# Kernel optimization log

Hardware: AMD Instinct MI355X
Metric: run time of the kernel (lower is better)

## Reference

```python
import jax, jax.numpy as jnp
import numpy as np

G = 16                 # grid side -> 4096 voxels
N_GRID = G ** 3
N_NODES = 4096         # protein nodes
DEG = 256              # node neighbors per grid voxel
HID = 64               # MPNN hidden == ResNet in_channels
NUM_CLASSES = 20
BN = np.float32(1.0 / np.sqrt(1.0 + 1e-5))  # eval-mode BatchNorm3d (mean=0, var=1, gamma=1, beta=0)


def _lin(key, fi, fo):
    return jax.random.normal(key, (fi, fo), jnp.float32) * (fi ** -0.5)


def _cw(key, o, i, k):
    return jax.random.normal(key, (o, i, k, k, k), jnp.float32) * ((i * k ** 3) ** -0.5)


def setup_inputs() -> dict:
    key = jax.random.key(0)
    ks = jax.random.split(key, 32)
    n_edges = N_GRID * DEG
    # every grid voxel receives exactly DEG messages (bincount never zero)
    edge_i = jax.random.randint(ks[0], (n_edges,), 0, N_NODES, dtype=jnp.int32)
    edge_j = jnp.repeat(jnp.arange(N_GRID, dtype=jnp.int32), DEG)
    edge_index = jnp.stack([edge_i, edge_j])  # [2, E]

    node_embedding = jax.random.normal(ks[1], (N_NODES, HID), jnp.float32)
    node_pos = jax.random.uniform(ks[2], (N_NODES, 3), jnp.float32)
    gx = (jnp.arange(G, dtype=jnp.float32) + 0.5) / G
    gd, gh, gw = jnp.meshgrid(gx, gx, gx, indexing='ij')
    grid_pos = jnp.stack([gd, gh, gw], -1).reshape(N_GRID, 3)

    z = lambda n: jnp.zeros((n,), jnp.float32)
    return {
        'node_embedding': node_embedding, 'node_pos': node_pos,
        'grid_pos': grid_pos, 'edge_index': edge_index,
        # MPNN edge / message / update MLPs
        'ew1': _lin(ks[3], 6, HID), 'eb1': z(HID), 'ew2': _lin(ks[4], HID, HID), 'eb2': z(HID),
        'mw1': _lin(ks[5], 2 * HID, HID), 'mb1': z(HID), 'mw2': _lin(ks[6], HID, HID), 'mb2': z(HID),
        'uw1': _lin(ks[7], HID, HID), 'ub1': z(HID), 'uw2': _lin(ks[8], HID, HID), 'ub2': z(HID),
        # ResNet3D: 3 Blocks (conv3 a, conv3 b, conv5 shortcut) with channels 64->64, 64->128, 128->256
        'c1a': _cw(ks[9], 64, 64, 3), 'c1b': _cw(ks[10], 64, 64, 3), 'c1s': _cw(ks[11], 64, 64, 5),
        'c2a': _cw(ks[12], 128, 64, 3), 'c2b': _cw(ks[13], 128, 128, 3), 'c2s': _cw(ks[14], 128, 64, 5),
        'c3a': _cw(ks[15], 256, 128, 3), 'c3b': _cw(ks[16], 256, 256, 3), 'c3s': _cw(ks[17], 256, 128, 5),
        'fcw': _lin(ks[18], 256, NUM_CLASSES), 'fcb': z(NUM_CLASSES),
    }


def _mlp(x, w1, b1, w2, b2):
    return jax.nn.silu(x @ w1 + b1) @ w2 + b2


def _conv(x, w, p):
    return jax.lax.conv_general_dilated(
        x, w, window_strides=(1, 1, 1), padding=[(p, p)] * 3,
        dimension_numbers=('NCDHW', 'OIDHW', 'NCDHW'))


def _block(x, wa, wb, ws):
    out = jax.nn.relu(_conv(x, wa, 1) * BN)
    out = _conv(out, wb, 1) * BN
    sc = _conv(x, ws, 2) * BN
    return jax.nn.relu(out + sc)


def reference(node_embedding, node_pos, grid_pos, edge_index,
              ew1, eb1, ew2, eb2, mw1, mb1, mw2, mb2, uw1, ub1, uw2, ub2,
              c1a, c1b, c1s, c2a, c2b, c2s, c3a, c3b, c3s, fcw, fcb):
    i, j = edge_index[0], edge_index[1]
    # ---- MPNN: gather, edge MLP, message MLP, scatter-mean, update MLP ----
    edge_attr = jnp.concatenate([node_pos[i], grid_pos[j]], axis=-1)        # [E, 6]
    pos_emb = _mlp(edge_attr, ew1, eb1, ew2, eb2)                           # [E, H]
    msg = _mlp(jnp.concatenate([node_embedding[i], pos_emb], -1),
               mw1, mb1, mw2, mb2)                                          # [E, H]
    agg = jax.ops.segment_sum(msg, j, num_segments=N_GRID)                  # [N_GRID, H]
    cnt = jax.ops.segment_sum(jnp.ones((msg.shape[0],), msg.dtype), j,
                              num_segments=N_GRID)
    grid_feat = _mlp(agg / cnt[:, None], uw1, ub1, uw2, ub2)                # [N_GRID, H]
    # ---- ResNet3D over the grid volume ----
    x = grid_feat.T.reshape(1, HID, G, G, G) * BN                           # instance_norm1 (eval BN)
    x = _block(x, c1a, c1b, c1s)
    x = _block(x, c2a, c2b, c2s)
    x = _block(x, c3a, c3b, c3s)
    pooled = jnp.max(x, axis=(2, 3, 4))                                     # max_pool3d(kernel=spatial)
    return pooled @ fcw + fcb                                               # [1, NUM_CLASSES]
```

## Files before the change

kernel.cpp:

```cpp
#include <hip/hip_runtime.h>
#include <math.h>

#define BN_S 0.9999950000374997f

typedef _Float16 half8 __attribute__((ext_vector_type(8)));
typedef float f32x4 __attribute__((ext_vector_type(4)));

__device__ __forceinline__ float silu_f(float x) {
    return __fdividef(x, 1.0f + __expf(-x));
}

__device__ __forceinline__ void gld16(const void* g, void* l) {
    __builtin_amdgcn_global_load_lds(
        (const __attribute__((address_space(1))) void*)g,
        (__attribute__((address_space(3))) void*)l, 16, 0, 0);
}

__global__ __launch_bounds__(64) void prep_w_k(
    const float* __restrict__ ew2, const float* __restrict__ mw1,
    const float* __restrict__ mw2, const float* __restrict__ uw1,
    const float* __restrict__ mb2, const float* __restrict__ ub1,
    float* __restrict__ W_mu, float* __restrict__ b_mu,
    _Float16* __restrict__ wemt_h, _Float16* __restrict__ wemt_l)
{
    const int k = blockIdx.x, c = threadIdx.x;
    float s = 0.f;
    for (int m = 0; m < 64; m++) s = fmaf(ew2[k*64 + m], mw1[(64 + m)*64 + c], s);
    {
        const int q = k >> 5, kg = (k >> 3) & 3, jj = k & 7;
        const int sl = q*256 + c*4 + kg;
        const int p = sl ^ ((sl >> 3) & 7);
        const _Float16 h = (_Float16)s;
        const _Float16 l = (_Float16)(s - (float)h);
        wemt_h[p*8 + jj] = h;
        wemt_l[p*8 + jj] = l;
    }
    float s2 = 0.f;
    for (int m = 0; m < 64; m++) s2 = fmaf(mw2[k*64 + m], uw1[m*64 + c], s2);
    W_mu[k*64 + c] = s2;
    if (k == 0) {
        float s3 = ub1[c];
        for (int m = 0; m < 64; m++) s3 = fmaf(mb2[m], uw1[m*64 + c], s3);
        b_mu[c] = s3;
    }
}

__global__ __launch_bounds__(64) void prep_nodes_k(
    const float* __restrict__ node_embedding, const float* __restrict__ node_pos,
    const float* __restrict__ grid_pos, const float* __restrict__ ew1,
    const float* __restrict__ eb1, const float* __restrict__ mw1,
    const float* __restrict__ mb1, const float* __restrict__ eb2,
    float* __restrict__ a_node, float* __restrict__ g_vox, float* __restrict__ n_node)
{
    const int v = blockIdx.x, c = threadIdx.x;
    const float p0 = node_pos[v*3], p1 = node_pos[v*3 + 1], p2 = node_pos[v*3 + 2];
    a_node[v*64 + c] = fmaf(p0, ew1[c], fmaf(p1, ew1[64 + c], fmaf(p2, ew1[128 + c], eb1[c])));
    const float q0 = grid_pos[v*3], q1 = grid_pos[v*3 + 1], q2 = grid_pos[v*3 + 2];
    g_vox[v*64 + c] = fmaf(q0, ew1[192 + c], fmaf(q1, ew1[256 + c], q2 * ew1[320 + c]));
    float s = mb1[c];
    for (int k = 0; k < 64; k++) s = fmaf(node_embedding[v*64 + k], mw1[k*64 + c], s);
    for (int k = 0; k < 64; k++) s = fmaf(eb2[k], mw1[(64 + k)*64 + c], s);
    n_node[v*64 + c] = s;
}

template<int K3, int NCOG, int NCH>
__global__ __launch_bounds__(256) void wsplit_k(
    const float* __restrict__ w, _Float16* __restrict__ dh, _Float16* __restrict__ dl,
    int CI)
{
    __shared__ float s[32*K3];
    const int co = blockIdx.x, cig = blockIdx.y, t = threadIdx.x;
    const float* src = w + ((size_t)co*CI + cig*32)*K3;
    for (int m = t; m < 32*K3; m += 256) s[m] = src[m];
    __syncthreads();
    const int coG = co >> 6, col = co & 63;
    for (int m = t; m < 32*K3; m += 256) {
        const int tap = m >> 5, cil = m & 31;
        const float x = s[cil*K3 + tap];
        const _Float16 h = (_Float16)x;
        const _Float16 l = (_Float16)(x - (float)h);
        const int b = cil >> 3, jj = cil & 7;
        const int sl = col*4 + b;
        const int p = sl ^ ((sl >> 3) & 7);
        const size_t base = ((size_t)(tap*NCOG + coG)*NCH + cig) * 2048;
        dh[base + p*8 + jj] = h;
        dl[base + p*8 + jj] = l;
    }
}

__global__ __launch_bounds__(256) void edge_kernel(
    const int* __restrict__ edge_i,
    const float* __restrict__ a_node, const float* __restrict__ g_vox,
    const float* __restrict__ n_node,
    const _Float16* __restrict__ wemt_h, const _Float16* __restrict__ wemt_l,
    const float* __restrict__ W_mu, const float* __restrict__ b_mu,
    const float* __restrict__ uw2, const float* __restrict__ ub2,
    _Float16* __restrict__ x0h, _Float16* __restrict__ x0l)
{
    __shared__ __align__(16) _Float16 sAh[4096], sAl[4096];
    __shared__ __align__(16) _Float16 sBh[4096], sBl[4096];
    __shared__ float sV1[64], sV2[64];

    const int j = blockIdx.x, t = threadIdx.x;
    const int lane = t & 63, wv = t >> 6, ln15 = lane & 15, kg = lane >> 4;
    const int ebase = j << 8;

    gld16(wemt_h + t*8, &sAh[t*8]);
    gld16(wemt_h + 2048 + t*8, &sAh[2048 + t*8]);
    gld16(wemt_l + t*8, &sAl[t*8]);
    gld16(wemt_l + 2048 + t*8, &sAl[2048 + t*8]);

    const int r = t >> 2, sub = t & 3;
    float gv[16];
    #pragma unroll
    for (int m = 0; m < 16; m++) gv[m] = g_vox[j*64 + sub*16 + m];

    asm volatile("s_waitcnt vmcnt(0)" ::: "memory");
    __syncthreads();

    float psum[4] = {0.f, 0.f, 0.f, 0.f};

    for (int T = 0; T < 4; T++) {
        {
            const int i = edge_i[ebase + T*64 + r];
            float s1[16];
            #pragma unroll
            for (int m = 0; m < 16; m++)
                s1[m] = silu_f(a_node[i*64 + sub*16 + m] + gv[m]);
            half8 h0, l0, h1, l1;
            #pragma unroll
            for (int m = 0; m < 8; m++) {
                h0[m] = (_Float16)s1[m];
                l0[m] = (_Float16)(s1[m] - (float)h0[m]);
                h1[m] = (_Float16)s1[8 + m];
                l1[m] = (_Float16)(s1[8 + m] - (float)h1[m]);
            }
            const int q = sub >> 1, kg0 = (sub & 1) * 2;
            const int slot0 = (q*4 + kg0)*64 + r;
            *(half8*)&sBh[slot0*8] = h0; *(half8*)&sBl[slot0*8] = l0;
            *(half8*)&sBh[(slot0 + 64)*8] = h1; *(half8*)&sBl[(slot0 + 64)*8] = l1;
        }
        __syncthreads();
        #pragma unroll
        for (int eF = 0; eF < 4; eF++) {
            const int e = eF*16 + ln15;
            const int ie = edge_i[ebase + T*64 + e];
            f32x4 acc;
            {
                const float4 nv = *(const float4*)&n_node[(size_t)ie*64 + wv*16 + kg*4];
                acc[0] = nv.x; acc[1] = nv.y; acc[2] = nv.z; acc[3] = nv.w;
            }
            #pragma unroll
            for (int q = 0; q < 2; q++) {
                const int sa = q*256 + (wv*16 + ln15)*4 + kg;
                const int pa = sa ^ ((sa >> 3) & 7);
                const half8 Ah = *(const half8*)&sAh[pa*8];
                const half8 Al = *(const half8*)&sAl[pa*8];
                const int sb = ((q*4 + kg)*64 + e)*8;
                const half8 Bh = *(const half8*)&sBh[sb];
                const half8 Bl = *(const half8*)&sBl[sb];
                acc = __builtin_amdgcn_mfma_f32_16x16x32_f16(Ah, Bh, acc, 0, 0, 0);
                acc = __builtin_amdgcn_mfma_f32_16x16x32_f16(Ah, Bl, acc, 0, 0, 0);
                acc = __builtin_amdgcn_mfma_f32_16x16x32_f16(Al, Bh, acc, 0, 0, 0);
            }
            #pragma unroll
            for (int rg = 0; rg < 4; rg++) psum[rg] += silu_f(acc[rg]);
        }
        __syncthreads();
    }

    #pragma unroll
    for (int rg = 0; rg < 4; rg++) {
        float v = psum[rg];
        v += __shfl_xor(v, 1, 64); v += __shfl_xor(v, 2, 64);
        v += __shfl_xor(v, 4, 64); v += __shfl_xor(v, 8, 64);
        psum[rg] = v;
    }
    if (ln15 == 0) {
        #pragma unroll
        for (int rg = 0; rg < 4; rg++)
            sV1[wv*16 + kg*4 + rg] = psum[rg] * (1.0f / 256.0f);
    }
    __syncthreads();
    if (t < 64) {
        float h = b_mu[t];
        for (int k = 0; k < 64; k++) h = fmaf(sV1[k], W_mu[k*64 + t], h);
        sV2[t] = silu_f(h);
    }
    __syncthreads();
    if (t < 64) {
        float g = ub2[t];
        for (int k = 0; k < 64; k++) g = fmaf(sV2[k], uw2[k*64 + t], g);
        const float val = g * BN_S;
        const _Float16 hh = (_Float16)val;
        const _Float16 ll = (_Float16)(val - (float)hh);
        const int c = t, zz = j >> 8, v = j & 255;
        const size_t a16 = ((size_t)((c >> 5)*16 + zz)*1024 + ((c >> 3) & 3)*256 + v)*8 + (c & 7);
        x0h[a16] = hh; x0l[a16] = ll;
    }
}

template<int KK, int CI, int NCOG, int CIS>
__global__ __launch_bounds__(256) void conv_mfma_k(
    const _Float16* __restrict__ xh, const _Float16* __restrict__ xl,
    const _Float16* __restrict__ wh, const _Float16* __restrict__ wl,
    float* __restrict__ slab)
{
    constexpr int P = KK/2, K2 = KK*KK, NCH = CI/32, NCHS = NCH/CIS, CO = NCOG*64;
    const int d0 = blockIdx.x, coG = blockIdx.y;
    const int cis = blockIdx.z / KK, kd = blockIdx.z % KK;
    const int t = threadIdx.x;
    const int lane = t & 63, wv = t >> 6;
    const int ln15 = lane & 15, kg = lane >> 4;

    float* sout = slab + ((size_t)blockIdx.z*CO + coG*64)*4096 + d0*256;
    const int z = d0 + kd - P;
    if ((unsigned)z >= 16u) {
        for (int m = t; m < 64*256; m += 256)
            sout[(size_t)(m >> 8)*4096 + (m & 255)] = 0.f;
        return;
    }

    __shared__ __align__(16) _Float16 sXh[2][8192];
    __shared__ __align__(16) _Float16 sXl[2][8192];
    __shared__ __align__(16) _Float16 zb[8];
    if (t < 8) zb[t] = (_Float16)0.f;

    int aoff[4];
    #pragma unroll
    for (int cf = 0; cf < 4; cf++) {
        const int s = (cf*16 + ln15)*4 + kg;
        aoff[cf] = (s ^ ((s >> 3) & 7)) * 8;
    }

    auto stage_X = [&](int xb, int ch) {
        const size_t b16 = ((size_t)ch*16 + z) * 8192;
        #pragma unroll
        for (int q = 0; q < 4; q++) {
            gld16(xh + b16 + (q*256 + t)*8, &sXh[xb][(q*256 + t)*8]);
            gld16(xl + b16 + (q*256 + t)*8, &sXl[xb][(q*256 + t)*8]);
        }
    };
    auto loadA = [&](int ch, int t2, half8* Ah, half8* Al) {
        const size_t b = ((size_t)((kd*K2 + t2)*NCOG + coG)*NCH + ch) * 2048;
        #pragma unroll
        for (int cf = 0; cf < 4; cf++) {
            Ah[cf] = *(const half8*)&wh[b + aoff[cf]];
            Al[cf] = *(const half8*)&wl[b + aoff[cf]];
        }
    };

    f32x4 acc[4][4];
    #pragma unroll
    for (int a = 0; a < 4; a++)
        #pragma unroll
        for (int b = 0; b < 4; b++)
            #pragma unroll
            for (int r2 = 0; r2 < 4; r2++) acc[a][b][r2] = 0.f;

    const int ch0 = cis * NCHS;
    half8 nAh[4], nAl[4];
    stage_X(0, ch0);
    loadA(ch0, 0, nAh, nAl);
    asm volatile("s_waitcnt vmcnt(0)" ::: "memory");
    __syncthreads();

    for (int cc = 0; cc < NCHS; cc++) {
        const int ch = ch0 + cc, xb = cc & 1;
        if (cc + 1 < NCHS) stage_X(xb ^ 1, ch + 1);
        for (int t2 = 0; t2 < K2; t2++) {
            half8 cAh[4], cAl[4];
            #pragma unroll
            for (int cf = 0; cf < 4; cf++) { cAh[cf] = nAh[cf]; cAl[cf] = nAl[cf]; }
            if (t2 + 1 < K2)          loadA(ch, t2 + 1, nAh, nAl);
            else if (cc + 1 < NCHS)   loadA(ch + 1, 0, nAh, nAl);

            const int kh = t2 / KK, kw = t2 % KK;
            __builtin_amdgcn_s_setprio(1);
            #pragma unroll
            for (int f = 0; f < 4; f++) {
                const int h_in = wv*4 + f + kh - P;
                if ((unsigned)h_in < 16u) {
                    const int w_in = ln15 + kw - P;
                    const bool ok = (unsigned)w_in < 16u;
                    const int slot = ok ? (kg*256 + h_in*16 + w_in) : 0;
                    const half8 Bh = ok ? *(const half8*)&sXh[xb][slot*8] : *(const half8*)zb;
                    const half8 Bl = ok ? *(const half8*)&sXl[xb][slot*8] : *(const half8*)zb;
                    #pragma unroll
                    for (int cf = 0; cf < 4; cf++) {
                        acc[cf][f] = __builtin_amdgcn_mfma_f32_16x16x32_f16(cAh[cf], Bh, acc[cf][f], 0, 0, 0);
                        acc[cf][f] = __builtin_amdgcn_mfma_f32_16x16x32_f16(cAh[cf], Bl, acc[cf][f], 0, 0, 0);
                        acc[cf][f] = __builtin_amdgcn_mfma_f32_16x16x32_f16(cAl[cf], Bh, acc[cf][f], 0, 0, 0);
                    }
                }
            }
            __builtin_amdgcn_s_setprio(0);
        }
        __syncthreads();
    }

    #pragma unroll
    for (int cf = 0; cf < 4; cf++)
        #pragma unroll
        for (int f = 0; f < 4; f++)
            #pragma unroll
            for (int r2 = 0; r2 < 4; r2++)
                sout[(size_t)(cf*16 + kg*4 + r2)*4096 + wv*64 + f*16 + ln15] = acc[cf][f][r2];
}

template<int S, int RMODE, int OUT>
__global__ __launch_bounds__(256) void reduce_k(
    const float* __restrict__ pbuf, const float* __restrict__ addsrc,
    float* __restrict__ outf, _Float16* __restrict__ oh, _Float16* __restrict__ ol,
    int CO)
{
    const int z = blockIdx.x, c8 = blockIdx.y, v = threadIdx.x;
    float val[8];
    #pragma unroll
    for (int jj = 0; jj < 8; jj++) {
        const int c = c8*8 + jj;
        float a = 0.f;
        #pragma unroll
        for (int s = 0; s < S; s++)
            a += pbuf[((size_t)s*CO + c)*4096 + z*256 + v];
        a *= BN_S;
        if (RMODE == 3) a += addsrc[(size_t)c*4096 + z*256 + v];
        if (RMODE != 2) a = fmaxf(a, 0.f);
        val[jj] = a;
    }
    if (OUT == 0) {
        #pragma unroll
        for (int jj = 0; jj < 8; jj++)
            outf[(size_t)(c8*8 + jj)*4096 + z*256 + v] = val[jj];
    } else if (OUT == 1) {
        half8 hv, lv;
        #pragma unroll
        for (int jj = 0; jj < 8; jj++) {
            hv[jj] = (_Float16)val[jj];
            lv[jj] = (_Float16)(val[jj] - (float)hv[jj]);
        }
        const size_t a16 = ((size_t)((c8 >> 2)*16 + z)*1024 + (c8 & 3)*256 + v)*8;
        *(half8*)&oh[a16] = hv;
        *(half8*)&ol[a16] = lv;
    } else {
        __shared__ float sm[4][8];
        #pragma unroll
        for (int jj = 0; jj < 8; jj++) {
            float m = val[jj];
            m = fmaxf(m, __shfl_xor(m, 1, 64));  m = fmaxf(m, __shfl_xor(m, 2, 64));
            m = fmaxf(m, __shfl_xor(m, 4, 64));  m = fmaxf(m, __shfl_xor(m, 8, 64));
            m = fmaxf(m, __shfl_xor(m, 16, 64)); m = fmaxf(m, __shfl_xor(m, 32, 64));
            if ((v & 63) == 0) sm[v >> 6][jj] = m;
        }
        __syncthreads();
        if (v < 8) {
            const float m = fmaxf(fmaxf(sm[0][v], sm[1][v]), fmaxf(sm[2][v], sm[3][v]));
            outf[z*CO + c8*8 + v] = m;
        }
    }
}

__global__ __launch_bounds__(256) void fc_k(
    const float* __restrict__ pp, const float* __restrict__ fcw,
    const float* __restrict__ fcb, float* __restrict__ out)
{
    __shared__ float sp[256];
    const int t = threadIdx.x;
    float m = pp[t];
    for (int zz = 1; zz < 16; zz++) m = fmaxf(m, pp[zz*256 + t]);
    sp[t] = m;
    __syncthreads();
    if (t < 20) {
        float s = fcb[t];
        for (int c = 0; c < 256; c++) s = fmaf(sp[c], fcw[c*20 + t], s);
        out[t] = s;
    }
}

extern "C" void kernel_launch(void* const* d_in, const int* in_sizes, int n_in,
                              void* d_out, int out_size, void* d_ws, size_t ws_size,
                              hipStream_t stream)
{
    const float* node_embedding = (const float*)d_in[0];
    const float* node_pos       = (const float*)d_in[1];
    const float* grid_pos       = (const float*)d_in[2];
    const int*   edge_index     = (const int*)d_in[3];
    const float* ew1 = (const float*)d_in[4];
    const float* eb1 = (const float*)d_in[5];
    const float* ew2 = (const float*)d_in[6];
    const float* eb2 = (const float*)d_in[7];
    const float* mw1 = (const float*)d_in[8];
    const float* mb1 = (const float*)d_in[9];
    const float* mw2 = (const float*)d_in[10];
    const float* mb2 = (const float*)d_in[11];
    const float* uw1 = (const float*)d_in[12];
    const float* ub1 = (const float*)d_in[13];
    const float* uw2 = (const float*)d_in[14];
    const float* ub2 = (const float*)d_in[15];
    const float* c1a = (const float*)d_in[16];
    const float* c1b = (const float*)d_in[17];
    const float* c1s = (const float*)d_in[18];
    const float* c2a = (const float*)d_in[19];
    const float* c2b = (const float*)d_in[20];
    const float* c2s = (const float*)d_in[21];
    const float* c3a = (const float*)d_in[22];
    const float* c3b = (const float*)d_in[23];
    const float* c3s = (const float*)d_in[24];
    const float* fcw = (const float*)d_in[25];
    const float* fcb = (const float*)d_in[26];
    float* out = (float*)d_out;
    const int* edge_i = edge_index;

    float* ws = (float*)d_ws;
    float* a_node = ws;                ws += 262144;
    float* g_vox  = ws;                ws += 262144;
    float* n_node = ws;                ws += 262144;
    float* W_mu   = ws;                ws += 4096;
    float* b_mu   = ws;                ws += 64;
    _Float16* wemt_h = (_Float16*)ws;  ws += 2048;
    _Float16* wemt_l = (_Float16*)ws;  ws += 2048;
    _Float16* x0h = (_Float16*)ws;     ws += 131072;
    _Float16* x0l = (_Float16*)ws;     ws += 131072;
    _Float16* t2h = (_Float16*)ws;     ws += 262144;
    _Float16* t2l = (_Float16*)ws;     ws += 262144;
    _Float16* x2h = (_Float16*)ws;     ws += 262144;
    _Float16* x2l = (_Float16*)ws;     ws += 262144;
    _Float16* t3h = (_Float16*)ws;     ws += 524288;
    _Float16* t3l = (_Float16*)ws;     ws += 524288;
    float* u2 = ws;                    ws += 524288;
    float* u3 = ws;                    ws += 1048576;
    float* slab = ws;                  ws += 5242880;
    float* poolPart = ws;              ws += 4096;
    _Float16* wh = (_Float16*)ws;      ws += 4585472;
    _Float16* wl = (_Float16*)ws;      ws += 4585472;
    _Float16* t1h = (_Float16*)a_node;
    _Float16* t1l = (_Float16*)(a_node + 131072);
    float* u1 = g_vox;
    _Float16* x1h = (_Float16*)n_node;
    _Float16* x1l = (_Float16*)(n_node + 131072);

    _Float16* w1a_h = wh + 0;       _Float16* w1a_l = wl + 0;
    _Float16* w1b_h = wh + 110592;  _Float16* w1b_l = wl + 110592;
    _Float16* w1s_h = wh + 221184;  _Float16* w1s_l = wl + 221184;
    _Float16* w2a_h = wh + 733184;  _Float16* w2a_l = wl + 733184;
    _Float16* w2b_h = wh + 954368;  _Float16* w2b_l = wl + 954368;
    _Float16* w2s_h = wh + 1396736; _Float16* w2s_l = wl + 1396736;
    _Float16* w3a_h = wh + 2420736; _Float16* w3a_l = wl + 2420736;
    _Float16* w3b_h = wh + 3305472; _Float16* w3b_l = wl + 3305472;
    _Float16* w3s_h = wh + 5074944; _Float16* w3s_l = wl + 5074944;

    hipLaunchKernelGGL((wsplit_k<27,1,2>),  dim3(64,2),  dim3(256), 0, stream, c1a, w1a_h, w1a_l, 64);
    hipLaunchKernelGGL((wsplit_k<27,1,2>),  dim3(64,2),  dim3(256), 0, stream, c1b, w1b_h, w1b_l, 64);
    hipLaunchKernelGGL((wsplit_k<125,1,2>), dim3(64,2),  dim3(256), 0, stream, c1s, w1s_h, w1s_l, 64);
    hipLaunchKernelGGL((wsplit_k<27,2,2>),  dim3(128,2), dim3(256), 0, stream, c2a, w2a_h, w2a_l, 64);
    hipLaunchKernelGGL((wsplit_k<27,2,4>),  dim3(128,4), dim3(256), 0, stream, c2b, w2b_h, w2b_l, 128);
    hipLaunchKernelGGL((wsplit_k<125,2,2>), dim3(128,2), dim3(256), 0, stream, c2s, w2s_h, w2s_l, 64);
    hipLaunchKernelGGL((wsplit_k<27,4,4>),  dim3(256,4), dim3(256), 0, stream, c3a, w3a_h, w3a_l, 128);
    hipLaunchKernelGGL((wsplit_k<27,4,8>),  dim3(256,8), dim3(256), 0, stream, c3b, w3b_h, w3b_l, 256);
    hipLaunchKernelGGL((wsplit_k<125,4,4>), dim3(256,4), dim3(256), 0, stream, c3s, w3s_h, w3s_l, 128);

    hipLaunchKernelGGL(prep_w_k, dim3(64), dim3(64), 0, stream,
                       ew2, mw1, mw2, uw1, mb2, ub1, W_mu, b_mu, wemt_h, wemt_l);
    hipLaunchKernelGGL(prep_nodes_k, dim3(4096), dim3(64), 0, stream,
                       node_embedding, node_pos, grid_pos, ew1, eb1, mw1, mb1, eb2,
                       a_node, g_vox, n_node);
    hipLaunchKernelGGL(edge_kernel, dim3(4096), dim3(256), 0, stream,
                       edge_i, a_node, g_vox, n_node, wemt_h, wemt_l,
                       W_mu, b_mu, uw2, ub2, x0h, x0l);

    hipLaunchKernelGGL((conv_mfma_k<3,64,1,2>), dim3(16,1,6), dim3(256), 0, stream, x0h, x0l, w1a_h, w1a_l, slab);
    hipLaunchKernelGGL((reduce_k<6,1,1>), dim3(16,8), dim3(256), 0, stream, slab, (const float*)nullptr, (float*)nullptr, t1h, t1l, 64);
    hipLaunchKernelGGL((conv_mfma_k<3,64,1,2>), dim3(16,1,6), dim3(256), 0, stream, t1h, t1l, w1b_h, w1b_l, slab);
    hipLaunchKernelGGL((reduce_k<6,2,0>), dim3(16,8), dim3(256), 0, stream, slab, (const float*)nullptr, u1, (_Float16*)nullptr, (_Float16*)nullptr, 64);
    hipLaunchKernelGGL((conv_mfma_k<5,64,1,2>), dim3(16,1,10), dim3(256), 0, stream, x0h, x0l, w1s_h, w1s_l, slab);
    hipLaunchKernelGGL((reduce_k<10,3,1>), dim3(16,8), dim3(256), 0, stream, slab, u1, (float*)nullptr, x1h, x1l, 64);
    hipLaunchKernelGGL((conv_mfma_k<3,64,2,2>), dim3(16,2,6), dim3(256), 0, stream, x1h, x1l, w2a_h, w2a_l, slab);
    hipLaunchKernelGGL((reduce_k<6,1,1>), dim3(16,16), dim3(256), 0, stream, slab, (const float*)nullptr, (float*)nullptr, t2h, t2l, 128);
    hipLaunchKernelGGL((conv_mfma_k<3,128,2,2>), dim3(16,2,6), dim3(256), 0, stream, t2h, t2l, w2b_h, w2b_l, slab);
    hipLaunchKernelGGL((reduce_k<6,2,0>), dim3(16,16), dim3(256), 0, stream, slab, (const float*)nullptr, u2, (_Float16*)nullptr, (_Float16*)nullptr, 128);
    hipLaunchKernelGGL((conv_mfma_k<5,64,2,2>), dim3(16,2,10), dim3(256), 0, stream, x1h, x1l, w2s_h, w2s_l, slab);
    hipLaunchKernelGGL((reduce_k<10,3,1>), dim3(16,16), dim3(256), 0, stream, slab, u2, (float*)nullptr, x2h, x2l, 128);
    hipLaunchKernelGGL((conv_mfma_k<3,128,4,1>), dim3(16,4,3), dim3(256), 0, stream, x2h, x2l, w3a_h, w3a_l, slab);
    hipLaunchKernelGGL((reduce_k<3,1,1>), dim3(16,32), dim3(256), 0, stream, slab, (const float*)nullptr, (float*)nullptr, t3h, t3l, 256);
    hipLaunchKernelGGL((conv_mfma_k<3,256,4,1>), dim3(16,4,3), dim3(256), 0, stream, t3h, t3l, w3b_h, w3b_l, slab);
    hipLaunchKernelGGL((reduce_k<3,2,0>), dim3(16,32), dim3(256), 0, stream, slab, (const float*)nullptr, u3, (_Float16*)nullptr, (_Float16*)nullptr, 256);
    hipLaunchKernelGGL((conv_mfma_k<5,128,4,1>), dim3(16,4,5), dim3(256), 0, stream, x2h, x2l, w3s_h, w3s_l, slab);
    hipLaunchKernelGGL((reduce_k<5,3,2>), dim3(16,32), dim3(256), 0, stream, slab, u3, poolPart, (_Float16*)nullptr, (_Float16*)nullptr, 256);

    hipLaunchKernelGGL(fc_k, dim3(1), dim3(256), 0, stream, poolPart, fcw, fcb, out);

    (void)in_sizes; (void)n_in; (void)out_size; (void)ws_size;
}
```

Baseline: 529.7 us.

## Double-buffer weight and LDS activation fragments across taps in conv MFMA loop

Restructures the conv inner loop into a two-stage ping-pong: the weight fragments for the next tap are loaded from global memory and the activation fragments are read from LDS while the MFMA burst for the current tap runs. Previously the LDS reads happened inline before each MFMA group. It also adds a min-blocks-per-CU hint of 2 to the launch bounds, plus an explicit vmcnt wait before the barrier. The extra fragment buffers raise register pressure, and the occupancy hint could force spills.

Result: slower. 763.5 us (+44.1%).

```diff
diff --git a/kernel.cpp b/kernel.cpp
--- a/kernel.cpp
+++ b/kernel.cpp
@@ -201,7 +201,7 @@
 }
 
 template<int KK, int CI, int NCOG, int CIS>
-__global__ __launch_bounds__(256) void conv_mfma_k(
+__global__ __launch_bounds__(256, 2) void conv_mfma_k(
     const _Float16* __restrict__ xh, const _Float16* __restrict__ xl,
     const _Float16* __restrict__ wh, const _Float16* __restrict__ wl,
     float* __restrict__ slab)
@@ -249,6 +249,22 @@
             Al[cf] = *(const half8*)&wl[b + aoff[cf]];
         }
     };
+    auto loadB = [&](int t2, int xb, half8* Bh, half8* Bl) {
+        const int kh = t2 / KK, kw = t2 - kh*KK;
+        const int w_in = ln15 + kw - P;
+        const bool okw = (unsigned)w_in < 16u;
+        #pragma unroll
+        for (int f = 0; f < 4; f++) {
+            const int h_in = wv*4 + f + kh - P;
+            if ((unsigned)h_in < 16u) {
+                const int slot = kg*256 + h_in*16 + (okw ? w_in : 0);
+                const _Float16* ph = okw ? &sXh[xb][slot*8] : zb;
+                const _Float16* pl = okw ? &sXl[xb][slot*8] : zb;
+                Bh[f] = *(const half8*)ph;
+                Bl[f] = *(const half8*)pl;
+            }
+        }
+    };
 
     f32x4 acc[4][4];
     #pragma unroll
@@ -258,44 +274,61 @@
             #pragma unroll
             for (int r2 = 0; r2 < 4; r2++) acc[a][b][r2] = 0.f;
 
+    auto burst = [&](int t2, const half8* Bh, const half8* Bl,
+                     const half8* Ah, const half8* Al) {
+        const int kh = t2 / KK;
+        __builtin_amdgcn_s_setprio(1);
+        #pragma unroll
+        for (int f = 0; f < 4; f++) {
+            const int h_in = wv*4 + f + kh - P;
+            if ((unsigned)h_in < 16u) {
+                #pragma unroll
+                for (int cf = 0; cf < 4; cf++) {
+                    acc[cf][f] = __builtin_amdgcn_mfma_f32_16x16x32_f16(Ah[cf], Bh[f], acc[cf][f], 0, 0, 0);
+                    acc[cf][f] = __builtin_amdgcn_mfma_f32_16x16x32_f16(Ah[cf], Bl[f], acc[cf][f], 0, 0, 0);
+                    acc[cf][f] = __builtin_amdgcn_mfma_f32_16x16x32_f16(Al[cf], Bh[f], acc[cf][f], 0, 0, 0);
+                }
+            }
+        }
+        __builtin_amdgcn_s_setprio(0);
+    };
+
+    half8 A0h[4], A0l[4], A1h[4], A1l[4];
+    half8 B0h[4], B0l[4], B1h[4], B1l[4];
+
     const int ch0 = cis * NCHS;
-    half8 nAh[4], nAl[4];
     stage_X(0, ch0);
-    loadA(ch0, 0, nAh, nAl);
+    loadA(ch0, 0, A0h, A0l);
     asm volatile("s_waitcnt vmcnt(0)" ::: "memory");
     __syncthreads();
 
     for (int cc = 0; cc < NCHS; cc++) {
         const int ch = ch0 + cc, xb = cc & 1;
         if (cc + 1 < NCHS) stage_X(xb ^ 1, ch + 1);
-        for (int t2 = 0; t2 < K2; t2++) {
-            half8 cAh[4], cAl[4];
-            #pragma unroll
-            for (int cf = 0; cf < 4; cf++) { cAh[cf] = nAh[cf]; cAl[cf] = nAl[cf]; }
-            if (t2 + 1 < K2)          loadA(ch, t2 + 1, nAh, nAl);
-            else if (cc + 1 < NCHS)   loadA(ch + 1, 0, nAh, nAl);
-
-            const int kh = t2 / KK, kw = t2 % KK;
-            __builtin_amdgcn_s_setprio(1);
-            #pragma unroll
-            for (int f = 0; f < 4; f++) {
-                const int h_in = wv*4 + f + kh - P;
-                if ((unsigned)h_in < 16u) {
-                    const int w_in = ln15 + kw - P;
-                    const bool ok = (unsigned)w_in < 16u;
-                    const int slot = ok ? (kg*256 + h_in*16 + w_in) : 0;
-                    const half8 Bh = ok ? *(const half8*)&sXh[xb][slot*8] : *(const half8*)zb;
-                    const half8 Bl = ok ? *(const half8*)&sXl[xb][slot*8] : *(const half8*)zb;
-                    #pragma unroll
-                    for (int cf = 0; cf < 4; cf++) {
-                        acc[cf][f] = __builtin_amdgcn_mfma_f32_16x16x32_f16(cAh[cf], Bh, acc[cf][f], 0, 0, 0);
-                        acc[cf][f] = __builtin_amdgcn_mfma_f32_16x16x32_f16(cAh[cf], Bl, acc[cf][f], 0, 0, 0);
-                        acc[cf][f] = __builtin_amdgcn_mfma_f32_16x16x32_f16(cAl[cf], Bh, acc[cf][f], 0, 0, 0);
-                    }
-                }
-            }
-            __builtin_amdgcn_s_setprio(0);
-        }
+        loadB(0, xb, B0h, B0l);
+
+        int t2 = 0;
+        for (; t2 + 2 <= K2; t2 += 2) {
+            loadA(ch, t2 + 1, A1h, A1l);
+            loadB(t2 + 1, xb, B1h, B1l);
+            burst(t2, B0h, B0l, A0h, A0l);
+            if (t2 + 2 < K2) {
+                loadA(ch, t2 + 2, A0h, A0l);
+                loadB(t2 + 2, xb, B0h, B0l);
+            } else if (cc + 1 < NCHS) {
+                loadA(ch + 1, 0, A0h, A0l);
+            }
+            burst(t2 + 1, B1h, B1l, A1h, A1l);
+        }
+        if (t2 < K2) {
+            if (cc + 1 < NCHS) loadA(ch + 1, 0, A1h, A1l);
+            burst(t2, B0h, B0l, A0h, A0l);
+            if (cc + 1 < NCHS) {
+                #pragma unroll
+                for (int cf = 0; cf < 4; cf++) { A0h[cf] = A1h[cf]; A0l[cf] = A1l[cf]; }
+            }
+        }
+        asm volatile("s_waitcnt vmcnt(0)" ::: "memory");
         __syncthreads();
     }
 
```
